# Performance work log

Hardware: AMD Instinct MI355X
Metric: run time of the kernel (lower is better)

Reference implementation:

```python
import jax, jax.numpy as jnp
import numpy as np

IN_F, OUT_F, RANK, ALPHA, NUM_ADAPTERS = 1024, 1024, 8, 1.0, 8
B, S = 32, 1024
SCALE = ALPHA / RANK


def setup_inputs() -> dict:
    key = jax.random.key(0)
    k1, k2, k3, k4, k5, k6 = jax.random.split(key, 6)
    x = jax.random.normal(k1, (B, S, IN_F), dtype=jnp.float32)
    subject_id = jax.random.randint(k2, (B,), 0, NUM_ADAPTERS)
    # base linear: W [out,in], bias [out] (torch nn.Linear layout)
    W = jax.random.normal(k3, (OUT_F, IN_F), dtype=jnp.float32) * (1.0 / np.sqrt(IN_F))
    b = jax.random.normal(k4, (OUT_F,), dtype=jnp.float32) * 0.01
    # stacked LoRA weights: A [E, rank, in], Bw [E, out, rank]
    # (original inits Bw to zeros; randomized here so the LoRA path is exercised)
    A = jax.random.normal(k5, (NUM_ADAPTERS, RANK, IN_F), dtype=jnp.float32) * 0.02
    Bw = jax.random.normal(k6, (NUM_ADAPTERS, OUT_F, RANK), dtype=jnp.float32) * 0.02
    return {"x": x, "W": W, "b": b, "A": A, "Bw": Bw, "subject_id": subject_id}


def reference(x, W, b, A, Bw, subject_id):
    # base linear: [B,S,O]
    out = jnp.einsum("bsd,od->bso", x, W) + b
    # gather per-batch adapter weights (equivalent to the per-adapter mask loop)
    A_sel = A[subject_id]   # [B, rank, in]
    B_sel = Bw[subject_id]  # [B, out, rank]
    h = jnp.einsum("bsd,brd->bsr", x, A_sel)          # [B,S,rank]
    lora = jnp.einsum("bsr,bor->bso", h, B_sel) * SCALE  # [B,S,out]
    return out + lora
```

## Files before the change

### kernel.cpp

```cpp
#include <hip/hip_runtime.h>
#include <hip/hip_bf16.h>

typedef __bf16 bf16_t;
typedef bf16_t bf16x4 __attribute__((ext_vector_type(4)));
typedef bf16_t bf16x8 __attribute__((ext_vector_type(8)));
typedef float  f32x4  __attribute__((ext_vector_type(4)));

#define IN_F   1024
#define OUT_F  1024
#define RANK   8
#define NE     8
#define BATCH  32
#define SEQ    1024
#define M_TOT  (BATCH * SEQ)
#define SCALE  0.125f
#define NT     16

#define GLOAD_LDS16(g, l)                                                     \
  __builtin_amdgcn_global_load_lds(                                           \
      (const __attribute__((address_space(1))) void*)(g),                     \
      (__attribute__((address_space(3))) void*)(l), 16, 0, 0)

#define CFENCE asm volatile("" ::: "memory")
#define BAR()                                                                 \
  do { CFENCE; __builtin_amdgcn_s_barrier(); CFENCE; } while (0)
#define VMCNT(n) asm volatile("s_waitcnt vmcnt(" #n ")" ::: "memory")

__global__ __launch_bounds__(256) void prep(
    const float* __restrict__ W, const float* __restrict__ A,
    const float* __restrict__ Bw, const float* __restrict__ x,
    bf16_t* __restrict__ weff, bf16_t* __restrict__ xb) {
  const int bid = blockIdx.x;
  if (bid < NE * OUT_F) {
    const int e  = bid >> 10;
    const int o  = bid & 1023;
    const int d0 = threadIdx.x << 2;
    f32x4 acc = *(const f32x4*)(W + ((size_t)o << 10) + d0);
    const float* bwr = Bw + (((size_t)e << 10) + o) * RANK;
    const float* ab  = A + (((size_t)e * RANK) << 10) + d0;
#pragma unroll
    for (int r = 0; r < RANK; ++r) {
      const float s = SCALE * bwr[r];
      const f32x4 a4 = *(const f32x4*)(ab + ((size_t)r << 10));
      acc += s * a4;
    }
    bf16x4 ov;
#pragma unroll
    for (int j = 0; j < 4; ++j) ov[j] = (bf16_t)acc[j];
    *(bf16x4*)(weff + (((size_t)e << 10) + o) * IN_F + d0) = ov;
  } else {
    const int cb = bid - NE * OUT_F;
    int i = cb * 256 + threadIdx.x;
    const int stride = 2048 * 256;
    const int n4 = M_TOT * IN_F / 4;
    for (; i < n4; i += stride) {
      const f32x4 v = *(const f32x4*)(x + ((size_t)i << 2));
      bf16x4 o;
#pragma unroll
      for (int j = 0; j < 4; ++j) o[j] = (bf16_t)v[j];
      *(bf16x4*)(xb + ((size_t)i << 2)) = o;
    }
  }
}

__global__ __launch_bounds__(512, 2) void gemm256(
    const bf16_t* __restrict__ xb, const bf16_t* __restrict__ weff,
    const float* __restrict__ bias, const int* __restrict__ sid,
    float* __restrict__ out) {
  __shared__ bf16_t lds_a[2][2][8192];
  __shared__ bf16_t lds_b[2][2][8192];

  const int bid0 = blockIdx.x;
  const int wgid = ((bid0 & 7) << 6) + (bid0 >> 3);
  const int mb = wgid >> 2, nb = wgid & 3;
  const int m0 = mb << 8, n0 = nb << 8;
  const int e = sid[mb >> 2];

  const int tid = threadIdx.x;
  const int lane = tid & 63, wid = tid >> 6;
  const int wm = wid >> 2, wn = wid & 3;

  const bf16_t* agbase = xb + ((size_t)m0 << 10);
  const bf16_t* bgbase = weff + ((size_t)e << 20) + ((size_t)n0 << 10);

  int soff[2];
#pragma unroll
  for (int i = 0; i < 2; ++i) {
    const int r = (wid << 5) + (i << 4) + (lane >> 2);
    const int sg = (lane & 3) ^ ((r >> 1) & 3);
    soff[i] = (r << 10) + (sg << 3);
  }

  int aoff[8], boff[4];
#pragma unroll
  for (int mi = 0; mi < 8; ++mi) {
    const int r = (wm << 7) + (mi << 4) + (lane & 15);
    const int g = (lane >> 4) ^ ((r >> 1) & 3);
    aoff[mi] = (r << 5) + (g << 3);
  }
#pragma unroll
  for (int ni = 0; ni < 4; ++ni) {
    const int r = (wn << 6) + (ni << 4) + (lane & 15);
    const int g = (lane >> 4) ^ ((r >> 1) & 3);
    boff[ni] = (r << 5) + (g << 3);
  }

  f32x4 acc[8][4] = {};
  bf16x8 afq[4], bf0[4], bf1[4];

#define ASTG(kt, c, kh)                                                       \
  do {                                                                        \
    bf16_t* _d = &lds_a[c][kh][wid << 10];                                    \
    const int _kc = ((kt) << 6) + ((kh) << 5);                                \
    GLOAD_LDS16(agbase + _kc + soff[0], _d);                                  \
    GLOAD_LDS16(agbase + _kc + soff[1], _d + 512);                            \
  } while (0)

#define BSTG(kt, c, kh)                                                       \
  do {                                                                        \
    bf16_t* _d = &lds_b[c][kh][wid << 10];                                    \
    const int _kc = ((kt) << 6) + ((kh) << 5);                                \
    GLOAD_LDS16(bgbase + _kc + soff[0], _d);                                  \
    GLOAD_LDS16(bgbase + _kc + soff[1], _d + 512);                            \
  } while (0)

#define RDB(SET, c, kh)                                                       \
  do {                                                                        \
    const bf16_t* _bb = &lds_b[c][kh][0];                                     \
    _Pragma("unroll") for (int ni = 0; ni < 4; ++ni)                          \
        SET[ni] = *(const bf16x8*)(_bb + boff[ni]);                           \
  } while (0)

#define RDA(c, kh, mb_)                                                       \
  do {                                                                        \
    const bf16_t* _ab = &lds_a[c][kh][0];                                     \
    _Pragma("unroll") for (int q = 0; q < 4; ++q)                             \
        afq[q] = *(const bf16x8*)(_ab + aoff[(mb_) + q]);                     \
  } while (0)

#define MM(SET, mb_)                                                          \
  do {                                                                        \
    __builtin_amdgcn_s_setprio(1);                                            \
    _Pragma("unroll") for (int q = 0; q < 4; ++q)                             \
        _Pragma("unroll") for (int ni = 0; ni < 4; ++ni)                      \
            acc[(mb_) + q][ni] = __builtin_amdgcn_mfma_f32_16x16x32_bf16(     \
                afq[q], SET[ni], acc[(mb_) + q][ni], 0, 0, 0);                \
    __builtin_amdgcn_s_setprio(0);                                            \
  } while (0)

#define TILE(JV, C, DO_S1, DO_S234, WTAIL)                                    \
  do {                                                                        \
                                                                      \
    RDB(bf0, C, 0); RDA(C, 0, 0);                                             \
    if (DO_S1) ASTG((JV) + 1, 1 - (C), 1);                                    \
    BAR(); MM(bf0, 0); BAR();                                                 \
                                                                      \
    RDA(C, 0, 4);                                                             \
    if (DO_S234) BSTG((JV) + 2, C, 0);                                        \
    BAR(); MM(bf0, 4); BAR();                                                 \
                                                                      \
    RDB(bf1, C, 1); RDA(C, 1, 0);                                             \
    if (DO_S234) ASTG((JV) + 2, C, 0);                                        \
    BAR(); MM(bf1, 0); BAR();                                                 \
                                                                      \
    RDA(C, 1, 4);                                                             \
    if (DO_S234) BSTG((JV) + 2, C, 1);                                        \
    WTAIL;                                                                    \
    BAR(); MM(bf1, 4); BAR();                                                 \
  } while (0)

  ASTG(0, 0, 0); ASTG(0, 0, 1); BSTG(0, 0, 0); BSTG(0, 0, 1);
  BSTG(1, 1, 0); ASTG(1, 1, 0); BSTG(1, 1, 1);
  VMCNT(6);
  BAR();

  for (int jj = 0; jj < 7; ++jj) {
    const int j0 = jj << 1;
    TILE(j0, 0, 1, 1, VMCNT(6));
    TILE(j0 + 1, 1, 1, 1, VMCNT(6));
  }
  TILE(14, 0, 1, 0, VMCNT(0));
  TILE(15, 1, 0, 0, (void)0);

  const int R0 = m0 + (wm << 7);
  const int C0 = n0 + (wn << 6);
  const int crow = (lane >> 4) << 2;
  const int ccol = lane & 15;
#pragma unroll
  for (int ni = 0; ni < 4; ++ni) {
    const int col = C0 + (ni << 4) + ccol;
    const float bv = bias[col];
#pragma unroll
    for (int mi = 0; mi < 8; ++mi) {
      const int row = R0 + (mi << 4) + crow;
#pragma unroll
      for (int j2 = 0; j2 < 4; ++j2)
        out[((size_t)(row + j2) << 10) + col] = acc[mi][ni][j2] + bv;
    }
  }
#undef ASTG
#undef BSTG
#undef RDB
#undef RDA
#undef MM
#undef TILE
}

__global__ __launch_bounds__(256) void lora_naive(
    const float* __restrict__ x, const float* __restrict__ W,
    const float* __restrict__ bias, const float* __restrict__ A,
    const float* __restrict__ Bw, const int* __restrict__ sid,
    float* __restrict__ out) {
  const int m = blockIdx.x;
  const int e = sid[m >> 10];
  __shared__ float xs[IN_F];
  __shared__ float h[RANK];
  const int tid = threadIdx.x;
  for (int i = tid; i < IN_F; i += 256) xs[i] = x[((size_t)m << 10) + i];
  __syncthreads();
  if (tid < RANK) {
    float s = 0.f;
    const float* ar = A + (((size_t)e * RANK + tid) << 10);
    for (int d = 0; d < IN_F; ++d) s += xs[d] * ar[d];
    h[tid] = s * SCALE;
  }
  __syncthreads();
  for (int o = tid; o < OUT_F; o += 256) {
    const float* wr = W + ((size_t)o << 10);
    float s = 0.f;
    for (int d = 0; d < IN_F; ++d) s += xs[d] * wr[d];
    const float* bwr = Bw + (((size_t)e << 10) + o) * RANK;
    float l = 0.f;
#pragma unroll
    for (int r = 0; r < RANK; ++r) l += h[r] * bwr[r];
    out[((size_t)m << 10) + o] = s + bias[o] + l;
  }
}

extern "C" void kernel_launch(void* const* d_in, const int* in_sizes, int n_in,
                              void* d_out, int out_size, void* d_ws,
                              size_t ws_size, hipStream_t stream) {
  const float* x   = (const float*)d_in[0];
  const float* W   = (const float*)d_in[1];
  const float* b   = (const float*)d_in[2];
  const float* A   = (const float*)d_in[3];
  const float* Bw  = (const float*)d_in[4];
  const int*   sid = (const int*)d_in[5];
  float* out = (float*)d_out;

  const size_t weff_bytes = (size_t)NE * OUT_F * IN_F * 2;
  const size_t xb_bytes   = (size_t)M_TOT * IN_F * 2;

  if (ws_size >= weff_bytes + xb_bytes) {
    bf16_t* weff = (bf16_t*)d_ws;
    bf16_t* xb   = (bf16_t*)((char*)d_ws + weff_bytes);
    hipLaunchKernelGGL(prep, dim3(NE * OUT_F + 2048), dim3(256), 0, stream,
                       W, A, Bw, x, weff, xb);
    hipLaunchKernelGGL(gemm256, dim3((M_TOT / 256) * (OUT_F / 256)),
                       dim3(512), 0, stream, xb, weff, b, sid, out);
  } else {
    hipLaunchKernelGGL(lora_naive, dim3(M_TOT), dim3(256), 0, stream,
                       x, W, b, A, Bw, sid, out);
  }
}
```

Before: 141.1 us.

## Replace 256x256 GEMM tile with 128x128 tile and simpler double-buffered pipeline

```diff
diff --git a/kernel.cpp b/kernel.cpp
--- a/kernel.cpp
+++ b/kernel.cpp
@@ -63,22 +63,22 @@
   }
 }
 
-__global__ __launch_bounds__(512, 2) void gemm256(
+__global__ __launch_bounds__(256, 2) void gemm128(
     const bf16_t* __restrict__ xb, const bf16_t* __restrict__ weff,
     const float* __restrict__ bias, const int* __restrict__ sid,
     float* __restrict__ out) {
-  __shared__ bf16_t lds_a[2][2][8192];
-  __shared__ bf16_t lds_b[2][2][8192];
+  __shared__ bf16_t lds_a[2][2][4096];
+  __shared__ bf16_t lds_b[2][2][4096];
 
   const int bid0 = blockIdx.x;
-  const int wgid = ((bid0 & 7) << 6) + (bid0 >> 3);
-  const int mb = wgid >> 2, nb = wgid & 3;
-  const int m0 = mb << 8, n0 = nb << 8;
-  const int e = sid[mb >> 2];
+  const int wgid = ((bid0 & 7) << 8) + (bid0 >> 3);
+  const int mb = wgid >> 3, nb = wgid & 7;
+  const int m0 = mb << 7, n0 = nb << 7;
+  const int e = sid[mb >> 3];
 
   const int tid = threadIdx.x;
   const int lane = tid & 63, wid = tid >> 6;
-  const int wm = wid >> 2, wn = wid & 3;
+  const int wm = wid >> 1, wn = wid & 1;
 
   const bf16_t* agbase = xb + ((size_t)m0 << 10);
   const bf16_t* bgbase = weff + ((size_t)e << 20) + ((size_t)n0 << 10);
@@ -86,15 +86,15 @@
   int soff[2];
 #pragma unroll
   for (int i = 0; i < 2; ++i) {
-    const int r = (wid << 5) + (i << 4) + (lane >> 2);
-    const int sg = (lane & 3) ^ ((r >> 1) & 3);
+    const int r = (i << 6) + (tid >> 2);
+    const int sg = (tid & 3) ^ ((r >> 1) & 3);
     soff[i] = (r << 10) + (sg << 3);
   }
 
-  int aoff[8], boff[4];
-#pragma unroll
-  for (int mi = 0; mi < 8; ++mi) {
-    const int r = (wm << 7) + (mi << 4) + (lane & 15);
+  int aoff[4], boff[4];
+#pragma unroll
+  for (int mi = 0; mi < 4; ++mi) {
+    const int r = (wm << 6) + (mi << 4) + (lane & 15);
     const int g = (lane >> 4) ^ ((r >> 1) & 3);
     aoff[mi] = (r << 5) + (g << 3);
   }
@@ -105,84 +105,76 @@
     boff[ni] = (r << 5) + (g << 3);
   }
 
-  f32x4 acc[8][4] = {};
-  bf16x8 afq[4], bf0[4], bf1[4];
+  f32x4 acc[4][4] = {};
+  bf16x8 af[4], bf[4];
 
 #define ASTG(kt, c, kh)                                                       \
   do {                                                                        \
-    bf16_t* _d = &lds_a[c][kh][wid << 10];                                    \
+    bf16_t* _d = &lds_a[c][kh][wid << 9];                                     \
     const int _kc = ((kt) << 6) + ((kh) << 5);                                \
     GLOAD_LDS16(agbase + _kc + soff[0], _d);                                  \
-    GLOAD_LDS16(agbase + _kc + soff[1], _d + 512);                            \
+    GLOAD_LDS16(agbase + _kc + soff[1], _d + 2048);                           \
   } while (0)
 
 #define BSTG(kt, c, kh)                                                       \
   do {                                                                        \
-    bf16_t* _d = &lds_b[c][kh][wid << 10];                                    \
+    bf16_t* _d = &lds_b[c][kh][wid << 9];                                     \
     const int _kc = ((kt) << 6) + ((kh) << 5);                                \
     GLOAD_LDS16(bgbase + _kc + soff[0], _d);                                  \
-    GLOAD_LDS16(bgbase + _kc + soff[1], _d + 512);                            \
-  } while (0)
-
-#define RDB(SET, c, kh)                                                       \
-  do {                                                                        \
+    GLOAD_LDS16(bgbase + _kc + soff[1], _d + 2048);                           \
+  } while (0)
+
+#define RD(c, kh)                                                             \
+  do {                                                                        \
+    const bf16_t* _ab = &lds_a[c][kh][0];                                     \
     const bf16_t* _bb = &lds_b[c][kh][0];                                     \
+    _Pragma("unroll") for (int mi = 0; mi < 4; ++mi)                          \
+        af[mi] = *(const bf16x8*)(_ab + aoff[mi]);                            \
     _Pragma("unroll") for (int ni = 0; ni < 4; ++ni)                          \
-        SET[ni] = *(const bf16x8*)(_bb + boff[ni]);                           \
-  } while (0)
-
-#define RDA(c, kh, mb_)                                                       \
-  do {                                                                        \
-    const bf16_t* _ab = &lds_a[c][kh][0];                                     \
-    _Pragma("unroll") for (int q = 0; q < 4; ++q)                             \
-        afq[q] = *(const bf16x8*)(_ab + aoff[(mb_) + q]);                     \
-  } while (0)
-
-#define MM(SET, mb_)                                                          \
+        bf[ni] = *(const bf16x8*)(_bb + boff[ni]);                            \
+  } while (0)
+
+#define MM()                                                                  \
   do {                                                                        \
     __builtin_amdgcn_s_setprio(1);                                            \
-    _Pragma("unroll") for (int q = 0; q < 4; ++q)                             \
+    _Pragma("unroll") for (int mi = 0; mi < 4; ++mi)                          \
         _Pragma("unroll") for (int ni = 0; ni < 4; ++ni)                      \
-            acc[(mb_) + q][ni] = __builtin_amdgcn_mfma_f32_16x16x32_bf16(     \
-                afq[q], SET[ni], acc[(mb_) + q][ni], 0, 0, 0);                \
+            acc[mi][ni] = __builtin_amdgcn_mfma_f32_16x16x32_bf16(            \
+                af[mi], bf[ni], acc[mi][ni], 0, 0, 0);                        \
     __builtin_amdgcn_s_setprio(0);                                            \
   } while (0)
 
-#define TILE(JV, C, DO_S1, DO_S234, WTAIL)                                    \
-  do {                                                                        \
-                                                                      \
-    RDB(bf0, C, 0); RDA(C, 0, 0);                                             \
-    if (DO_S1) ASTG((JV) + 1, 1 - (C), 1);                                    \
-    BAR(); MM(bf0, 0); BAR();                                                 \
-                                                                      \
-    RDA(C, 0, 4);                                                             \
-    if (DO_S234) BSTG((JV) + 2, C, 0);                                        \
-    BAR(); MM(bf0, 4); BAR();                                                 \
-                                                                      \
-    RDB(bf1, C, 1); RDA(C, 1, 0);                                             \
-    if (DO_S234) ASTG((JV) + 2, C, 0);                                        \
-    BAR(); MM(bf1, 0); BAR();                                                 \
-                                                                      \
-    RDA(C, 1, 4);                                                             \
-    if (DO_S234) BSTG((JV) + 2, C, 1);                                        \
-    WTAIL;                                                                    \
-    BAR(); MM(bf1, 4); BAR();                                                 \
-  } while (0)
-
-  ASTG(0, 0, 0); ASTG(0, 0, 1); BSTG(0, 0, 0); BSTG(0, 0, 1);
-  BSTG(1, 1, 0); ASTG(1, 1, 0); BSTG(1, 1, 1);
-  VMCNT(6);
+#define TILE(JV, C)                                                           \
+  do {                                                                        \
+                                                                 \
+    RD(C, 0);                                                                 \
+    ASTG((JV) + 1, 1 - (C), 0); BSTG((JV) + 1, 1 - (C), 0);                   \
+    VMCNT(4); BAR();                                                          \
+    MM();                                                                     \
+                                                                 \
+    RD(C, 1);                                                                 \
+    ASTG((JV) + 1, 1 - (C), 1); BSTG((JV) + 1, 1 - (C), 1);                   \
+    VMCNT(4); BAR();                                                          \
+    MM();                                                                     \
+  } while (0)
+
+  ASTG(0, 0, 0); BSTG(0, 0, 0);
+  ASTG(0, 0, 1); BSTG(0, 0, 1);
+  VMCNT(4);
   BAR();
 
   for (int jj = 0; jj < 7; ++jj) {
-    const int j0 = jj << 1;
-    TILE(j0, 0, 1, 1, VMCNT(6));
-    TILE(j0 + 1, 1, 1, 1, VMCNT(6));
-  }
-  TILE(14, 0, 1, 0, VMCNT(0));
-  TILE(15, 1, 0, 0, (void)0);
-
-  const int R0 = m0 + (wm << 7);
+    TILE(2 * jj, 0);
+    TILE(2 * jj + 1, 1);
+  }
+  TILE(14, 0);
+  RD(1, 0);
+  VMCNT(0); BAR();
+  MM();
+  RD(1, 1);
+  MM();
+
+  const int R0 = m0 + (wm << 6);
   const int C0 = n0 + (wn << 6);
   const int crow = (lane >> 4) << 2;
   const int ccol = lane & 15;
@@ -191,7 +183,7 @@
     const int col = C0 + (ni << 4) + ccol;
     const float bv = bias[col];
 #pragma unroll
-    for (int mi = 0; mi < 8; ++mi) {
+    for (int mi = 0; mi < 4; ++mi) {
       const int row = R0 + (mi << 4) + crow;
 #pragma unroll
       for (int j2 = 0; j2 < 4; ++j2)
@@ -200,8 +192,7 @@
   }
 #undef ASTG
 #undef BSTG
-#undef RDB
-#undef RDA
+#undef RD
 #undef MM
 #undef TILE
 }
@@ -256,8 +247,8 @@
     bf16_t* xb   = (bf16_t*)((char*)d_ws + weff_bytes);
     hipLaunchKernelGGL(prep, dim3(NE * OUT_F + 2048), dim3(256), 0, stream,
                        W, A, Bw, x, weff, xb);
-    hipLaunchKernelGGL(gemm256, dim3((M_TOT / 256) * (OUT_F / 256)),
-                       dim3(512), 0, stream, xb, weff, b, sid, out);
+    hipLaunchKernelGGL(gemm128, dim3((M_TOT / 128) * (OUT_F / 128)),
+                       dim3(256), 0, stream, xb, weff, b, sid, out);
   } else {
     hipLaunchKernelGGL(lora_naive, dim3(M_TOT), dim3(256), 0, stream,
                        x, W, b, A, Bw, sid, out);
```

New measurement: 140.0 us. Within noise of the previous version (-0.8%).
